# Optimization experiments

Hardware: AMD Instinct MI355X
Metric: run time of the kernel (lower is better)

## Reference

```python
import jax, jax.numpy as jnp
import numpy as np

DIM = 512
BATCH = 65536


def setup_inputs() -> dict:
    key = jax.random.key(0)
    k1, k2 = jax.random.split(key)
    pq = jax.random.normal(k1, (BATCH, 2 * DIM), dtype=jnp.float32)
    A = jax.random.normal(k2, (DIM, DIM), dtype=jnp.float32)
    return {"pq": pq, "A": A}


def reference(pq, A):
    # up_or_low == 'up': pterm_i = (A + A^T) @ q_i, qterm = 0
    # npq = [p + pterm, q]
    S = A + A.T  # symmetric (dim, dim)
    p = pq[:, :DIM]
    q = pq[:, DIM:]
    # torch.mv(S, q_i) for every row i  ==  q @ S.T  (single batched matvec/GEMM)
    pterm = jnp.einsum("bd,ed->be", q, S)
    return jnp.concatenate([p + pterm, q], axis=-1)
```

## Files before the change

### kernel.cpp

```cpp
#include <hip/hip_runtime.h>

#define DIM 512
#define BATCH 65536
#define BM 32
#define THREADS 512
#define TILES 4
#define NBLK (BATCH / (BM * TILES))

typedef float f32x4 __attribute__((ext_vector_type(4)));
typedef float f32x16 __attribute__((ext_vector_type(16)));
typedef __bf16 bf16x8 __attribute__((ext_vector_type(8)));

__device__ __forceinline__ unsigned f2bf(float f) {
    unsigned u = __float_as_uint(f);
    return (u + 0x7FFFu + ((u >> 16) & 1u)) >> 16;
}

__global__ void prep_Sfrag(const float* __restrict__ A, unsigned short* __restrict__ Sf) {
    int idx = blockIdx.x * 256 + threadIdx.x;
    int lane = idx & 63;
    int np   = (idx >> 6) & 15;
    int k0   = idx >> 10;
    int n     = np * 32 + (lane & 31);
    int kbase = k0 * 16 + (lane >> 5) * 8;
    unsigned short tmp[8];
    #pragma unroll
    for (int j = 0; j < 8; ++j) {
        int k = kbase + j;
        tmp[j] = (unsigned short)f2bf(A[n * DIM + k] + A[k * DIM + n]);
    }
    *(uint4*)(Sf + (size_t)idx * 8) = *(const uint4*)tmp;
}

__global__ __launch_bounds__(THREADS, 4)
void gemm_kernel(const float* __restrict__ pq,
                 const unsigned short* __restrict__ Sf,
                 float* __restrict__ out) {
    __shared__ __align__(16) unsigned short qh[2][BM * 256];
    __shared__ float sc[BM * 256];
    const int tid  = threadIdx.x;
    const int wid  = tid >> 6;
    const int lane = tid & 63;
    const int row  = lane & 31;
    const int khalf = lane >> 5;
    const int rb = blockIdx.x * (BM * TILES);
    const unsigned short* Sfp = Sf + ((size_t)(wid * 2) * 64 + lane) * 8;
    const int col0 = wid * 64 + row;
    (void)col0;

    f32x4 stg[4];

    auto issue_loads = [&](int ph) {
        int tile = ph >> 1, half = ph & 1;
        #pragma unroll
        for (int i = 0; i < 2; ++i) {
            int slot = i * THREADS + tid;
            int r = slot >> 5, c8 = slot & 31;
            size_t g = (size_t)(rb + tile * BM + r) * 1024 + 512 + half * 256 + c8 * 8;
            stg[2*i]   = __builtin_nontemporal_load((const f32x4*)(pq + g));
            stg[2*i+1] = __builtin_nontemporal_load((const f32x4*)(pq + g + 4));
        }
    };
    auto write_back = [&](int ph) {
        int tile = ph >> 1, half = ph & 1;
        unsigned short* dst = qh[ph & 1];
        #pragma unroll
        for (int i = 0; i < 2; ++i) {
            int slot = i * THREADS + tid;
            int r = slot >> 5, c8 = slot & 31;
            size_t g = (size_t)(rb + tile * BM + r) * 1024 + 512 + half * 256 + c8 * 8;
            __builtin_nontemporal_store(stg[2*i],   (f32x4*)(out + g));
            __builtin_nontemporal_store(stg[2*i+1], (f32x4*)(out + g + 4));
            unsigned u0 = f2bf(stg[2*i].x)   | (f2bf(stg[2*i].y)   << 16);
            unsigned u1 = f2bf(stg[2*i].z)   | (f2bf(stg[2*i].w)   << 16);
            unsigned u2 = f2bf(stg[2*i+1].x) | (f2bf(stg[2*i+1].y) << 16);
            unsigned u3 = f2bf(stg[2*i+1].z) | (f2bf(stg[2*i+1].w) << 16);
            int b = r * 512 + ((c8 * 16) ^ ((r & 7) << 4));
            *(uint4*)((char*)dst + b) = make_uint4(u0, u1, u2, u3);
        }
    };
    auto khalf_loop = [&](int ph, f32x16& acc0, f32x16& acc1) {
        int half = ph & 1;
        const unsigned short* buf = qh[ph & 1];
        const unsigned short* sp = Sfp + (size_t)(half * 16) * 8192;
        bf16x8 b0_c = *(const bf16x8*)(sp);
        bf16x8 b1_c = *(const bf16x8*)(sp + 512);
        #pragma unroll
        for (int k = 0; k < 16; ++k) {
            bf16x8 b0_n, b1_n;
            if (k < 15) {
                b0_n = *(const bf16x8*)(sp + (size_t)(k + 1) * 8192);
                b1_n = *(const bf16x8*)(sp + (size_t)(k + 1) * 8192 + 512);
            }
            int b = row * 512 + ((k * 32 + khalf * 16) ^ ((row & 7) << 4));
            bf16x8 a = *(const bf16x8*)((const char*)buf + b);
            acc0 = __builtin_amdgcn_mfma_f32_32x32x16_bf16(a, b0_c, acc0, 0, 0, 0);
            acc1 = __builtin_amdgcn_mfma_f32_32x32x16_bf16(a, b1_c, acc1, 0, 0, 0);
            if (k < 15) { b0_c = b0_n; b1_c = b1_n; }
        }
    };
    auto epilogue = [&](int tile, const f32x16& acc0, const f32x16& acc1) {
        int tb = rb + tile * BM;
        #pragma unroll
        for (int pass = 0; pass < 2; ++pass) {
            const f32x16& ac = pass ? acc1 : acc0;
            #pragma unroll
            for (int reg = 0; reg < 16; ++reg) {
                int r = (reg & 3) + 8 * (reg >> 2) + 4 * khalf;
                sc[r * 256 + wid * 32 + row] = ac[reg];
            }
            __syncthreads();
            #pragma unroll
            for (int j = 0; j < 4; ++j) {
                int c = tid + j * 512;
                int r = c >> 6, cc = c & 63;
                int gcol = (cc >> 3) * 64 + (cc & 7) * 4 + pass * 32;
                size_t g = (size_t)(tb + r) * 1024 + gcol;
                f32x4 v  = *(const f32x4*)(sc + r * 256 + cc * 4);
                f32x4 pv = __builtin_nontemporal_load((const f32x4*)(pq + g));
                __builtin_nontemporal_store(pv + v, (f32x4*)(out + g));
            }
            __syncthreads();
        }
    };

    f32x16 acc0, acc1;
    issue_loads(0);
    write_back(0);
    __syncthreads();

    for (int ph = 0; ph < 2 * TILES; ++ph) {
        if ((ph & 1) == 0) { acc0 = f32x16{}; acc1 = f32x16{}; }
        if (ph + 1 < 2 * TILES) issue_loads(ph + 1);
        khalf_loop(ph, acc0, acc1);
        if (ph + 1 < 2 * TILES) write_back(ph + 1);
        __syncthreads();
        if (ph & 1) epilogue(ph >> 1, acc0, acc1);
    }
}

extern "C" void kernel_launch(void* const* d_in, const int* in_sizes, int n_in,
                              void* d_out, int out_size, void* d_ws, size_t ws_size,
                              hipStream_t stream) {
    const float* pq = (const float*)d_in[0];
    const float* A  = (const float*)d_in[1];
    float* out = (float*)d_out;
    unsigned short* Sf = (unsigned short*)d_ws;

    prep_Sfrag<<<128, 256, 0, stream>>>(A, Sf);
    gemm_kernel<<<NBLK, THREADS, 0, stream>>>(pq, Sf, out);
}
```

Before: 131.7 us.

## Load q operand fragments directly from global memory instead of LDS staging

Removes the bf16 LDS staging buffer for q. Each wave now loads its MFMA A-operand fragments straight from global fp32 pq, converts them to bf16 in registers, and software-prefetches one k-step ahead. The q copy to the output is still done with separate cached loads and nontemporal stores. This cuts LDS traffic and the per-phase barriers, but every wave now re-reads the same q rows from global/L2, so global load traffic rises and the cross-phase load overlap is lost.

```diff
diff --git a/kernel.cpp b/kernel.cpp
--- a/kernel.cpp
+++ b/kernel.cpp
@@ -36,7 +36,6 @@
 void gemm_kernel(const float* __restrict__ pq,
                  const unsigned short* __restrict__ Sf,
                  float* __restrict__ out) {
-    __shared__ __align__(16) unsigned short qh[2][BM * 256];
     __shared__ float sc[BM * 256];
     const int tid  = threadIdx.x;
     const int wid  = tid >> 6;
@@ -45,58 +44,53 @@
     const int khalf = lane >> 5;
     const int rb = blockIdx.x * (BM * TILES);
     const unsigned short* Sfp = Sf + ((size_t)(wid * 2) * 64 + lane) * 8;
-    const int col0 = wid * 64 + row;
-    (void)col0;
+
+    const int r0 = tid >> 5, c8 = tid & 31;
+    const int r1 = r0 + 16;
 
     f32x4 stg[4];
 
-    auto issue_loads = [&](int ph) {
-        int tile = ph >> 1, half = ph & 1;
-        #pragma unroll
-        for (int i = 0; i < 2; ++i) {
-            int slot = i * THREADS + tid;
-            int r = slot >> 5, c8 = slot & 31;
-            size_t g = (size_t)(rb + tile * BM + r) * 1024 + 512 + half * 256 + c8 * 8;
-            stg[2*i]   = __builtin_nontemporal_load((const f32x4*)(pq + g));
-            stg[2*i+1] = __builtin_nontemporal_load((const f32x4*)(pq + g + 4));
-        }
+    auto issue_q = [&](int t, int half) {
+        size_t g0 = (size_t)(rb + t * BM + r0) * 1024 + 512 + half * 256 + c8 * 8;
+        size_t g1 = (size_t)(rb + t * BM + r1) * 1024 + 512 + half * 256 + c8 * 8;
+        stg[0] = *(const f32x4*)(pq + g0);
+        stg[1] = *(const f32x4*)(pq + g0 + 4);
+        stg[2] = *(const f32x4*)(pq + g1);
+        stg[3] = *(const f32x4*)(pq + g1 + 4);
     };
-    auto write_back = [&](int ph) {
-        int tile = ph >> 1, half = ph & 1;
-        unsigned short* dst = qh[ph & 1];
-        #pragma unroll
-        for (int i = 0; i < 2; ++i) {
-            int slot = i * THREADS + tid;
-            int r = slot >> 5, c8 = slot & 31;
-            size_t g = (size_t)(rb + tile * BM + r) * 1024 + 512 + half * 256 + c8 * 8;
-            __builtin_nontemporal_store(stg[2*i],   (f32x4*)(out + g));
-            __builtin_nontemporal_store(stg[2*i+1], (f32x4*)(out + g + 4));
-            unsigned u0 = f2bf(stg[2*i].x)   | (f2bf(stg[2*i].y)   << 16);
-            unsigned u1 = f2bf(stg[2*i].z)   | (f2bf(stg[2*i].w)   << 16);
-            unsigned u2 = f2bf(stg[2*i+1].x) | (f2bf(stg[2*i+1].y) << 16);
-            unsigned u3 = f2bf(stg[2*i+1].z) | (f2bf(stg[2*i+1].w) << 16);
-            int b = r * 512 + ((c8 * 16) ^ ((r & 7) << 4));
-            *(uint4*)((char*)dst + b) = make_uint4(u0, u1, u2, u3);
-        }
+    auto store_q = [&](int t, int half) {
+        size_t g0 = (size_t)(rb + t * BM + r0) * 1024 + 512 + half * 256 + c8 * 8;
+        size_t g1 = (size_t)(rb + t * BM + r1) * 1024 + 512 + half * 256 + c8 * 8;
+        __builtin_nontemporal_store(stg[0], (f32x4*)(out + g0));
+        __builtin_nontemporal_store(stg[1], (f32x4*)(out + g0 + 4));
+        __builtin_nontemporal_store(stg[2], (f32x4*)(out + g1));
+        __builtin_nontemporal_store(stg[3], (f32x4*)(out + g1 + 4));
     };
-    auto khalf_loop = [&](int ph, f32x16& acc0, f32x16& acc1) {
-        int half = ph & 1;
-        const unsigned short* buf = qh[ph & 1];
+    auto khalf_direct = [&](int t, int half, f32x16& acc0, f32x16& acc1) {
         const unsigned short* sp = Sfp + (size_t)(half * 16) * 8192;
+        const float* qp = pq + (size_t)(rb + t * BM + row) * 1024 + 512
+                             + half * 256 + khalf * 8;
+        f32x4 alo_c = *(const f32x4*)(qp);
+        f32x4 ahi_c = *(const f32x4*)(qp + 4);
         bf16x8 b0_c = *(const bf16x8*)(sp);
         bf16x8 b1_c = *(const bf16x8*)(sp + 512);
         #pragma unroll
         for (int k = 0; k < 16; ++k) {
-            bf16x8 b0_n, b1_n;
+            f32x4 alo_n, ahi_n; bf16x8 b0_n, b1_n;
             if (k < 15) {
-                b0_n = *(const bf16x8*)(sp + (size_t)(k + 1) * 8192);
-                b1_n = *(const bf16x8*)(sp + (size_t)(k + 1) * 8192 + 512);
+                alo_n = *(const f32x4*)(qp + (k + 1) * 16);
+                ahi_n = *(const f32x4*)(qp + (k + 1) * 16 + 4);
+                b0_n  = *(const bf16x8*)(sp + (size_t)(k + 1) * 8192);
+                b1_n  = *(const bf16x8*)(sp + (size_t)(k + 1) * 8192 + 512);
             }
-            int b = row * 512 + ((k * 32 + khalf * 16) ^ ((row & 7) << 4));
-            bf16x8 a = *(const bf16x8*)((const char*)buf + b);
+            bf16x8 a;
+            a[0] = (__bf16)alo_c[0]; a[1] = (__bf16)alo_c[1];
+            a[2] = (__bf16)alo_c[2]; a[3] = (__bf16)alo_c[3];
+            a[4] = (__bf16)ahi_c[0]; a[5] = (__bf16)ahi_c[1];
+            a[6] = (__bf16)ahi_c[2]; a[7] = (__bf16)ahi_c[3];
             acc0 = __builtin_amdgcn_mfma_f32_32x32x16_bf16(a, b0_c, acc0, 0, 0, 0);
             acc1 = __builtin_amdgcn_mfma_f32_32x32x16_bf16(a, b1_c, acc1, 0, 0, 0);
-            if (k < 15) { b0_c = b0_n; b1_c = b1_n; }
+            if (k < 15) { alo_c = alo_n; ahi_c = ahi_n; b0_c = b0_n; b1_c = b1_n; }
         }
     };
     auto epilogue = [&](int tile, const f32x16& acc0, const f32x16& acc1) {
@@ -125,17 +119,16 @@
     };
 
     f32x16 acc0, acc1;
-    issue_loads(0);
-    write_back(0);
-    __syncthreads();
-
-    for (int ph = 0; ph < 2 * TILES; ++ph) {
-        if ((ph & 1) == 0) { acc0 = f32x16{}; acc1 = f32x16{}; }
-        if (ph + 1 < 2 * TILES) issue_loads(ph + 1);
-        khalf_loop(ph, acc0, acc1);
-        if (ph + 1 < 2 * TILES) write_back(ph + 1);
-        __syncthreads();
-        if (ph & 1) epilogue(ph >> 1, acc0, acc1);
+    for (int t = 0; t < TILES; ++t) {
+        acc0 = f32x16{};
+        acc1 = f32x16{};
+        issue_q(t, 0);
+        khalf_direct(t, 0, acc0, acc1);
+        store_q(t, 0);
+        issue_q(t, 1);
+        khalf_direct(t, 1, acc0, acc1);
+        store_q(t, 1);
+        epilogue(t, acc0, acc1);
     }
 }
 
```

New measurement: 380.7 us. +189.1%, slower.
